# Kernel tuning notes

Measured on AMD Instinct MI355X. Metric: run time of the kernel, lower is better.

Reference implementation:

```python
import jax, jax.numpy as jnp
import numpy as np

K = 5
THRESHOLD = 0.1


def _l2norm(x, eps=1e-12):
    # matches torch.nn.functional.normalize(dim=-1)
    n = jnp.sqrt(jnp.sum(x * x, axis=-1, keepdims=True))
    return x / jnp.maximum(n, eps)


def setup_inputs() -> dict:
    key = jax.random.key(0)
    ks = jax.random.split(key, 5)
    B, CDD, HIS, L, LVL, H = 32, 5, 50, 32, 2, 256
    return {
        "cdd_repr": jax.random.normal(ks[0], (B, CDD, H), dtype=jnp.float32),
        "his_repr": jax.random.normal(ks[1], (B, HIS, H), dtype=jnp.float32),
        "his_embedding": jax.random.normal(ks[2], (B, HIS, L, LVL, H), dtype=jnp.float32),
        "his_attn_mask": jax.random.randint(ks[3], (B, HIS, L), 0, 2).astype(jnp.int32),
        # xavier-normal-ish init for the selection projection
        "W": jax.random.normal(ks[4], (H, H), dtype=jnp.float32) * np.float32(np.sqrt(2.0 / (H + H))),
        "b": jnp.zeros((H,), dtype=jnp.float32),
    }


def reference(cdd_repr, his_repr, his_embedding, his_attn_mask, W, b):
    # selection projection + L2 normalize
    c = _l2norm(cdd_repr @ W.T + b)           # [B, cdd, H]
    h = _l2norm(his_repr @ W.T + b)           # [B, his, H]
    # news-level attention scores
    attn = jnp.einsum("bcd,bhd->bch", c, h)   # [B, cdd, his]
    # top-k history selection (sorted descending, like torch.topk)
    vals, idx = jax.lax.top_k(attn, K)        # [B, cdd, k]
    # gather top-k history embeddings / masks per (batch, cdd)
    his_activated = jax.vmap(lambda e, i: e[i])(his_embedding, idx)   # [B, cdd, k, L, lvl, H]
    his_mask_activated = jax.vmap(lambda m, i: m[i])(his_attn_mask, idx)  # [B, cdd, k, L]
    # threshold mask + reweight (fused elementwise)
    w = jnp.where(vals < THRESHOLD, jnp.float32(0.0), vals)
    his_activated = his_activated * w[..., None, None, None]
    return his_activated, his_mask_activated
```

## Files before the change

kernel.cpp:

```cpp
#include <hip/hip_runtime.h>
#include <hip/hip_bf16.h>

#define B_    32
#define CDD_  5
#define HIS_  50
#define L_    32
#define LVL_  2
#define H_    256
#define K_    5
#define NCDD  (B_*CDD_)
#define NHIS  (B_*HIS_)
#define NROWS (NCDD + NHIS)
#define SLAB  (L_*LVL_*H_)
#define OUT0  ((size_t)NCDD*K_*SLAB)

#define ROWS_A 8

__global__ __launch_bounds__(256) void proj_norm_kernel(
    const float* __restrict__ cdd, const float* __restrict__ his,
    const float* __restrict__ Wm, const float* __restrict__ bias,
    float* __restrict__ Y)
{
    __shared__ float part[ROWS_A][4];
    __shared__ float inv[ROWS_A];
    const int t = threadIdx.x;
    const int r0 = blockIdx.x * ROWS_A;

    const float4* xr[ROWS_A];
    #pragma unroll
    for (int r = 0; r < ROWS_A; ++r) {
        int row = r0 + r;
        const float* p = (row < NCDD) ? (cdd + (size_t)row * H_)
                                      : (his + (size_t)(row - NCDD) * H_);
        xr[r] = (const float4*)p;
    }

    float acc[ROWS_A];
    #pragma unroll
    for (int r = 0; r < ROWS_A; ++r) acc[r] = 0.f;

    const float4* wrow = (const float4*)(Wm + (size_t)t * H_);

    #pragma unroll 4
    for (int ch = 0; ch < H_ / 8; ++ch) {
        float4 w0 = wrow[2*ch];
        float4 w1 = wrow[2*ch + 1];
        #pragma unroll
        for (int r = 0; r < ROWS_A; ++r) {
            float4 xa = xr[r][2*ch];
            float4 xb = xr[r][2*ch + 1];
            acc[r] += w0.x*xa.x + w0.y*xa.y + w0.z*xa.z + w0.w*xa.w
                    + w1.x*xb.x + w1.y*xb.y + w1.z*xb.z + w1.w*xb.w;
        }
    }

    const float bt = bias[t];
    float y[ROWS_A], ss[ROWS_A];
    #pragma unroll
    for (int r = 0; r < ROWS_A; ++r) { y[r] = acc[r] + bt; ss[r] = y[r]*y[r]; }

    const int wave = t >> 6, lane = t & 63;
    #pragma unroll
    for (int off = 32; off; off >>= 1) {
        #pragma unroll
        for (int r = 0; r < ROWS_A; ++r) ss[r] += __shfl_down(ss[r], off);
    }
    if (lane == 0) {
        #pragma unroll
        for (int r = 0; r < ROWS_A; ++r) part[r][wave] = ss[r];
    }
    __syncthreads();
    if (t < ROWS_A) {
        float s = part[t][0] + part[t][1] + part[t][2] + part[t][3];
        inv[t] = 1.0f / fmaxf(sqrtf(s), 1e-12f);
    }
    __syncthreads();

    float* yp = Y + (size_t)r0 * H_ + t;
    #pragma unroll
    for (int r = 0; r < ROWS_A; ++r) yp[r * H_] = y[r] * inv[r];
}

__global__ __launch_bounds__(256) void attn_topk_kernel(
    const float* __restrict__ Y, const int* __restrict__ mask,
    int* __restrict__ idx_ws, float* __restrict__ w_ws,
    float* __restrict__ mask_out)
{
    const int bc = blockIdx.x;
    const int b  = bc / CDD_;
    __shared__ float cs[H_];
    __shared__ float scores[HIS_];
    __shared__ int   sidx[K_];
    const int t = threadIdx.x;

    cs[t] = Y[(size_t)bc * H_ + t];
    __syncthreads();

    const int wave = t >> 6, lane = t & 63;
    for (int h = wave; h < HIS_; h += 4) {
        const float4* hv = (const float4*)(Y + (size_t)(NCDD + b * HIS_ + h) * H_);
        float4 x  = hv[lane];
        float4 c4 = ((float4*)cs)[lane];
        float p = x.x*c4.x + x.y*c4.y + x.z*c4.z + x.w*c4.w;
        #pragma unroll
        for (int off = 32; off; off >>= 1) p += __shfl_down(p, off);
        if (lane == 0) scores[h] = p;
    }
    __syncthreads();

    if (wave == 0) {
        float v = (lane < HIS_) ? scores[lane] : -1e30f;
        #pragma unroll
        for (int k = 0; k < K_; ++k) {
            float mv = v; int mi = lane;
            #pragma unroll
            for (int off = 32; off; off >>= 1) {
                float ov = __shfl_xor(mv, off);
                int   oi = __shfl_xor(mi, off);
                if (ov > mv || (ov == mv && oi < mi)) { mv = ov; mi = oi; }
            }
            if (lane == 0) {
                sidx[k] = mi;
                idx_ws[bc * K_ + k] = mi;
                w_ws[bc * K_ + k]   = (mv < 0.1f) ? 0.0f : mv;
            }
            if (lane == mi) v = -1e30f;
        }
    }
    __syncthreads();

    if (t < K_ * L_) {
        int k = t / L_, l = t % L_;
        mask_out[((size_t)bc * K_ + k) * L_ + l] =
            (float)mask[((size_t)(b * HIS_ + sidx[k])) * L_ + l];
    }
}

__global__ __launch_bounds__(256) void gather_scale_kernel(
    const float* __restrict__ emb, const int* __restrict__ idx_ws,
    const float* __restrict__ w_ws, float* __restrict__ out)
{
    const int gb    = blockIdx.x;
    const int slice = gb & 7;
    const int bck   = gb >> 3;
    const int bc    = bck / K_;
    const int b     = bc / CDD_;
    const int i     = idx_ws[bck];
    const float w   = w_ws[bck];

    const float4* src = (const float4*)(emb + (size_t)(b * HIS_ + i) * SLAB);
    float4*       dst = (float4*)(out + (size_t)bck * SLAB);
    const int base = slice * 512 + threadIdx.x;

    float4 v0 = src[base];
    float4 v1 = src[base + 256];
    v0.x *= w; v0.y *= w; v0.z *= w; v0.w *= w;
    v1.x *= w; v1.y *= w; v1.z *= w; v1.w *= w;
    dst[base]       = v0;
    dst[base + 256] = v1;
}

extern "C" void kernel_launch(void* const* d_in, const int* in_sizes, int n_in,
                              void* d_out, int out_size, void* d_ws, size_t ws_size,
                              hipStream_t stream) {
    const float* cdd  = (const float*)d_in[0];
    const float* his  = (const float*)d_in[1];
    const float* emb  = (const float*)d_in[2];
    const int*   mask = (const int*)  d_in[3];
    const float* Wm   = (const float*)d_in[4];
    const float* bias = (const float*)d_in[5];
    float* out = (float*)d_out;

    float* Y      = (float*)d_ws;
    int*   idx_ws = (int*)  ((char*)d_ws + (size_t)NROWS*H_*4);
    float* w_ws   = (float*)((char*)d_ws + (size_t)NROWS*H_*4 + 800*4);

    proj_norm_kernel<<<NROWS / ROWS_A, 256, 0, stream>>>(cdd, his, Wm, bias, Y);
    attn_topk_kernel<<<NCDD, 256, 0, stream>>>(Y, mask, idx_ws, w_ws, out + OUT0);
    gather_scale_kernel<<<NCDD * K_ * 8, 256, 0, stream>>>(emb, idx_ws, w_ws, out);
}
```

Baseline: 220.2 us.

## Skip embedding reads for zero-weight slabs and stage projection inputs in LDS

The gather kernel now checks the thresholded weight first. If it is zero, it writes zeros and never reads the history embedding slab, which removes read traffic for every below-threshold top-k entry. The projection kernel now stages its 8 input rows in shared memory. Each thread computes two output columns for 4 rows, so the input rows are no longer reloaded from global memory by every thread. The zero shortcut assumes the embeddings hold only finite values, since NaN or Inf times zero would otherwise propagate.

Result: faster. 198.5 us (-9.9%).

```diff
diff --git a/kernel.cpp b/kernel.cpp
--- a/kernel.cpp
+++ b/kernel.cpp
@@ -21,64 +21,79 @@
     const float* __restrict__ Wm, const float* __restrict__ bias,
     float* __restrict__ Y)
 {
-    __shared__ float part[ROWS_A][4];
+    __shared__ float xs[ROWS_A][H_];
+    __shared__ float part[ROWS_A][2];
     __shared__ float inv[ROWS_A];
     const int t = threadIdx.x;
     const int r0 = blockIdx.x * ROWS_A;
 
-    const float4* xr[ROWS_A];
-    #pragma unroll
-    for (int r = 0; r < ROWS_A; ++r) {
-        int row = r0 + r;
-        const float* p = (row < NCDD) ? (cdd + (size_t)row * H_)
-                                      : (his + (size_t)(row - NCDD) * H_);
-        xr[r] = (const float4*)p;
-    }
-
-    float acc[ROWS_A];
-    #pragma unroll
-    for (int r = 0; r < ROWS_A; ++r) acc[r] = 0.f;
-
-    const float4* wrow = (const float4*)(Wm + (size_t)t * H_);
+    #pragma unroll
+    for (int j = t; j < ROWS_A * (H_/4); j += 256) {
+        int rr = j >> 6, cc = j & 63;
+        int row = r0 + rr;
+        const float* src = (row < NCDD) ? (cdd + (size_t)row * H_)
+                                        : (his + (size_t)(row - NCDD) * H_);
+        ((float4*)xs[rr])[cc] = ((const float4*)src)[cc];
+    }
+    __syncthreads();
+
+    const int wave = t >> 6, lane = t & 63;
+    const int rowHalf = wave >> 1;
+    const int colHalf = wave & 1;
+    const int c0 = colHalf * 128 + lane;
+    const int c1 = c0 + 64;
+
+    float acc0[4] = {0.f, 0.f, 0.f, 0.f};
+    float acc1[4] = {0.f, 0.f, 0.f, 0.f};
+    const float4* w0 = (const float4*)(Wm + (size_t)c0 * H_);
+    const float4* w1 = (const float4*)(Wm + (size_t)c1 * H_);
 
     #pragma unroll 4
-    for (int ch = 0; ch < H_ / 8; ++ch) {
-        float4 w0 = wrow[2*ch];
-        float4 w1 = wrow[2*ch + 1];
-        #pragma unroll
-        for (int r = 0; r < ROWS_A; ++r) {
-            float4 xa = xr[r][2*ch];
-            float4 xb = xr[r][2*ch + 1];
-            acc[r] += w0.x*xa.x + w0.y*xa.y + w0.z*xa.z + w0.w*xa.w
-                    + w1.x*xb.x + w1.y*xb.y + w1.z*xb.z + w1.w*xb.w;
+    for (int c = 0; c < H_ / 4; ++c) {
+        float4 wa = w0[c];
+        float4 wb = w1[c];
+        #pragma unroll
+        for (int r = 0; r < 4; ++r) {
+            float4 x = ((float4*)xs[rowHalf * 4 + r])[c];
+            acc0[r] += wa.x*x.x + wa.y*x.y + wa.z*x.z + wa.w*x.w;
+            acc1[r] += wb.x*x.x + wb.y*x.y + wb.z*x.z + wb.w*x.w;
         }
     }
 
-    const float bt = bias[t];
-    float y[ROWS_A], ss[ROWS_A];
-    #pragma unroll
-    for (int r = 0; r < ROWS_A; ++r) { y[r] = acc[r] + bt; ss[r] = y[r]*y[r]; }
-
-    const int wave = t >> 6, lane = t & 63;
+    const float bt0 = bias[c0];
+    const float bt1 = bias[c1];
+    float y0[4], y1[4], ss[4];
+    #pragma unroll
+    for (int r = 0; r < 4; ++r) {
+        y0[r] = acc0[r] + bt0;
+        y1[r] = acc1[r] + bt1;
+        ss[r] = y0[r]*y0[r] + y1[r]*y1[r];
+    }
+
     #pragma unroll
     for (int off = 32; off; off >>= 1) {
         #pragma unroll
-        for (int r = 0; r < ROWS_A; ++r) ss[r] += __shfl_down(ss[r], off);
+        for (int r = 0; r < 4; ++r) ss[r] += __shfl_down(ss[r], off);
     }
     if (lane == 0) {
         #pragma unroll
-        for (int r = 0; r < ROWS_A; ++r) part[r][wave] = ss[r];
+        for (int r = 0; r < 4; ++r) part[rowHalf * 4 + r][colHalf] = ss[r];
     }
     __syncthreads();
     if (t < ROWS_A) {
-        float s = part[t][0] + part[t][1] + part[t][2] + part[t][3];
+        float s = part[t][0] + part[t][1];
         inv[t] = 1.0f / fmaxf(sqrtf(s), 1e-12f);
     }
     __syncthreads();
 
-    float* yp = Y + (size_t)r0 * H_ + t;
-    #pragma unroll
-    for (int r = 0; r < ROWS_A; ++r) yp[r * H_] = y[r] * inv[r];
+    #pragma unroll
+    for (int r = 0; r < 4; ++r) {
+        const int gr = rowHalf * 4 + r;
+        const float iv = inv[gr];
+        float* yr = Y + (size_t)(r0 + gr) * H_;
+        yr[c0] = y0[r] * iv;
+        yr[c1] = y1[r] * iv;
+    }
 }
 
 __global__ __launch_bounds__(256) void attn_topk_kernel(
@@ -145,13 +160,20 @@
     const int bck   = gb >> 3;
     const int bc    = bck / K_;
     const int b     = bc / CDD_;
-    const int i     = idx_ws[bck];
     const float w   = w_ws[bck];
 
+    float4* dst = (float4*)(out + (size_t)bck * SLAB);
+    const int base = slice * 512 + threadIdx.x;
+
+    if (w == 0.0f) {
+        float4 z = make_float4(0.f, 0.f, 0.f, 0.f);
+        dst[base]       = z;
+        dst[base + 256] = z;
+        return;
+    }
+
+    const int i = idx_ws[bck];
     const float4* src = (const float4*)(emb + (size_t)(b * HIS_ + i) * SLAB);
-    float4*       dst = (float4*)(out + (size_t)bck * SLAB);
-    const int base = slice * 512 + threadIdx.x;
-
     float4 v0 = src[base];
     float4 v1 = src[base + 256];
     v0.x *= w; v0.y *= w; v0.z *= w; v0.w *= w;
```
